# Performance work log

Measured on AMD Instinct MI355X. Metric: run time of the kernel, lower is better.

Reference implementation:

```python
import jax, jax.numpy as jnp
import numpy as np

N_HEAD = 12

def setup_inputs() -> dict:
    key = jax.random.key(0)
    k1, k2, k3, k4, k5 = jax.random.split(key, 5)
    B, T, C = 16, 1024, 768
    s = 0.02
    return {
        "x": jax.random.normal(k1, (B, T, C), dtype=jnp.float32),
        "W_attn": jax.random.normal(k2, (C, 3 * C), dtype=jnp.float32) * s,
        "b_attn": jax.random.normal(k3, (3 * C,), dtype=jnp.float32) * s,
        "W_proj": jax.random.normal(k4, (C, C), dtype=jnp.float32) * s,
        "b_proj": jax.random.normal(k5, (C,), dtype=jnp.float32) * s,
    }

def reference(x, W_attn, b_attn, W_proj, b_proj):
    B, T, C = x.shape
    H = N_HEAD
    d = C // H
    qkv = x @ W_attn + b_attn                      # [B,T,3C]
    q, k, v = jnp.split(qkv, 3, axis=-1)
    # [B,H,T,d]
    q = q.reshape(B, T, H, d).transpose(0, 2, 1, 3)
    k = k.reshape(B, T, H, d).transpose(0, 2, 1, 3)
    v = v.reshape(B, T, H, d).transpose(0, 2, 1, 3)
    scale = 1.0 / jnp.sqrt(jnp.array(d, dtype=x.dtype))
    att = jnp.einsum('bhqd,bhkd->bhqk', q, k) * scale   # [B,H,T,T]
    causal = jnp.tril(jnp.ones((T, T), dtype=bool))
    att = jnp.where(causal[None, None], att, -jnp.inf)
    att = jax.nn.softmax(att, axis=-1)
    # dropout is identity in eval mode (p=0 for deterministic reference)
    y = jnp.einsum('bhqk,bhkd->bhqd', att, v)            # [B,H,T,d]
    y = y.transpose(0, 2, 1, 3).reshape(B, T, C)
    return y @ W_proj + b_proj
```

## Files before the change

### kernel.cpp

```cpp
#include <hip/hip_runtime.h>
#include <cstddef>


typedef __bf16 bf16_t;
typedef __bf16 bf16x4 __attribute__((ext_vector_type(4)));
typedef __bf16 bf16x8 __attribute__((ext_vector_type(8)));
typedef float  f32x4  __attribute__((ext_vector_type(4)));

#define MFMA16(a,b,c) __builtin_amdgcn_mfma_f32_16x16x32_bf16((a),(b),(c),0,0,0)
#define GLOAD16(gp, lp) \
  __builtin_amdgcn_global_load_lds((const __attribute__((address_space(1))) unsigned int*)(gp), \
                                   (__attribute__((address_space(3))) unsigned int*)(lp), 16, 0, 0)

#define SWZ(row, c) (((row) * 64) + ((((c) ^ ((row) & 7)) * 8)))

#define QSCALE 0.1803368801111f

__global__ __launch_bounds__(256)
void xcast_kernel(const float* __restrict__ in, bf16_t* __restrict__ out)
{
    const size_t i = ((size_t)blockIdx.x * 256 + threadIdx.x) * 4;
    float4 f = *(const float4*)(in + i);
    bf16x4 o = {(bf16_t)f.x, (bf16_t)f.y, (bf16_t)f.z, (bf16_t)f.w};
    *(bf16x4*)(out + i) = o;
}

__global__ __launch_bounds__(256)
void tcast_kernel(const float* __restrict__ in, bf16_t* __restrict__ out, int R, int Cn)
{
    __shared__ bf16_t tile[32][33];
    const int tx = threadIdx.x & 31, ty = threadIdx.x >> 5;
    const int c0 = blockIdx.x * 32, r0 = blockIdx.y * 32;
#pragma unroll
    for (int i = 0; i < 4; ++i)
        tile[ty + i*8][tx] = (bf16_t)in[(size_t)(r0 + ty + i*8) * Cn + c0 + tx];
    __syncthreads();
#pragma unroll
    for (int i = 0; i < 4; ++i)
        out[(size_t)(c0 + ty + i*8) * R + r0 + tx] = tile[tx][ty + i*8];
}

#define LGKM0() asm volatile("s_waitcnt lgkmcnt(0)" ::: "memory")
#define VMC(n)  asm volatile("s_waitcnt vmcnt(" #n ")" ::: "memory")
#define PBAR()  __builtin_amdgcn_s_barrier()
#define PRIO1() __builtin_amdgcn_s_setprio(1)
#define PRIO0() __builtin_amdgcn_s_setprio(0)

#define STAGE_HT(buf, kt, ht) do { \
    const int r0_ = w * 16 + (((ht) & 1) ? 128 : 0); \
    if ((ht) < 2) { \
        GLOAD16(WT + (size_t)(nt + r0_ + lr) * 768 + (kt) + lcs,     &Bs[buf][r0_ * 64]); \
        GLOAD16(WT + (size_t)(nt + r0_ + 8 + lr) * 768 + (kt) + lcs, &Bs[buf][(r0_ + 8) * 64]); \
    } else { \
        GLOAD16(Xb + (size_t)(mt + r0_ + lr) * 768 + (kt) + lcs,     &As[buf][r0_ * 64]); \
        GLOAD16(Xb + (size_t)(mt + r0_ + 8 + lr) * 768 + (kt) + lcs, &As[buf][(r0_ + 8) * 64]); \
    } \
} while (0)

#define RD_BX(dst, buf) do { \
    _Pragma("unroll") for (int j_ = 0; j_ < 4; ++j_) \
    _Pragma("unroll") for (int ks_ = 0; ks_ < 2; ++ks_) \
        (dst)[j_][ks_] = *(const bf16x8*)(&As[buf][SWZ(wc * 64 + j_ * 16 + lm, ks_ * 4 + lq)]); \
} while (0)

#define RD_AW(dst, buf, F0, NF) do { \
    _Pragma("unroll") for (int p_ = 0; p_ < (NF); ++p_) \
    _Pragma("unroll") for (int ks_ = 0; ks_ < 2; ++ks_) \
        (dst)[p_][ks_] = *(const bf16x8*)(&Bs[buf][SWZ(wr * 128 + ((F0) + p_) * 16 + lm, ks_ * 4 + lq)]); \
} while (0)

#define MFMA_Q(AW, BX, F0) do { \
    _Pragma("unroll") for (int ks_ = 0; ks_ < 2; ++ks_) \
    _Pragma("unroll") for (int p_ = 0; p_ < 2; ++p_) \
    _Pragma("unroll") for (int j_ = 0; j_ < 4; ++j_) \
        acc[(F0) + p_][j_] = MFMA16((AW)[p_][ks_], (BX)[j_][ks_], acc[(F0) + p_][j_]); \
} while (0)

__global__ __launch_bounds__(512)
void qkv_gemm8(const bf16_t* __restrict__ Xb, const bf16_t* __restrict__ WT,
               const float* __restrict__ bias,
               bf16_t* __restrict__ Qb, bf16_t* __restrict__ Kb, bf16_t* __restrict__ VT)
{
    __shared__ bf16_t As[2][256 * 64];
    __shared__ bf16_t Bs[2][256 * 64];
    const int tid = threadIdx.x;
    const int w = tid >> 6, l = tid & 63;
    const int lm = l & 15, lq = l >> 4;
    const int lr = l >> 3;
    const int lcs = ((l & 7) ^ lr) * 8;
    const int wr = w >> 2, wc = w & 3;

    const int g = blockIdx.x;
    const int gt = (g & 7) * 72 + (g >> 3);
    const int bm = gt / 9, bn = gt % 9;
    const int mt = bm * 256, nt = bn * 256;

    f32x4 acc[8][4];
    const f32x4 z4 = {0.f, 0.f, 0.f, 0.f};
#pragma unroll
    for (int i = 0; i < 8; ++i)
#pragma unroll
        for (int j = 0; j < 4; ++j) acc[i][j] = z4;

    bf16x8 bx0[4][2], bx1[4][2];
    bf16x8 aw0[2][2], aw12[4][2], aw3[2][2];

    STAGE_HT(0, 0, 0); STAGE_HT(0, 0, 1); STAGE_HT(0, 0, 2); STAGE_HT(0, 0, 3);
    STAGE_HT(1, 64, 0); STAGE_HT(1, 64, 1);
    VMC(4);
    PBAR();
    RD_BX(bx0, 0); RD_AW(aw0, 0, 0, 2);

#pragma unroll 1
    for (int it = 0; it < 5; ++it) {
        const int kv = it * 128 + 64, ku2 = kv + 64, kv2 = ku2 + 64;
        RD_AW(aw12, 0, 2, 4);
        STAGE_HT(1, kv, 2);
        PBAR(); LGKM0();
        PRIO1(); MFMA_Q(aw0, bx0, 0); PRIO0();
        PBAR();
        RD_AW(aw3, 0, 6, 2);
        STAGE_HT(1, kv, 3);
        PBAR(); LGKM0();
        PRIO1(); MFMA_Q(aw12, bx0, 2); PRIO0();
        PBAR();
        STAGE_HT(0, ku2, 0);
        PBAR();
        PRIO1(); MFMA_Q(&aw12[2], bx0, 4); PRIO0();
        VMC(2);
        PBAR();
        RD_BX(bx1, 1); RD_AW(aw0, 1, 0, 2);
        STAGE_HT(0, ku2, 1);
        PBAR(); LGKM0();
        PRIO1(); MFMA_Q(aw3, bx0, 6); PRIO0();
        PBAR();
        RD_AW(aw12, 1, 2, 4);
        STAGE_HT(0, ku2, 2);
        PBAR(); LGKM0();
        PRIO1(); MFMA_Q(aw0, bx1, 0); PRIO0();
        PBAR();
        RD_AW(aw3, 1, 6, 2);
        STAGE_HT(0, ku2, 3);
        PBAR(); LGKM0();
        PRIO1(); MFMA_Q(aw12, bx1, 2); PRIO0();
        PBAR();
        STAGE_HT(1, kv2, 0);
        PBAR();
        PRIO1(); MFMA_Q(&aw12[2], bx1, 4); PRIO0();
        VMC(2);
        PBAR();
        RD_BX(bx0, 0); RD_AW(aw0, 0, 0, 2);
        STAGE_HT(1, kv2, 1);
        PBAR(); LGKM0();
        PRIO1(); MFMA_Q(aw3, bx1, 6); PRIO0();
        PBAR();
    }

    RD_AW(aw12, 0, 2, 4);
    STAGE_HT(1, 704, 2);
    PBAR(); LGKM0();
    PRIO1(); MFMA_Q(aw0, bx0, 0); PRIO0();
    PBAR();
    RD_AW(aw3, 0, 6, 2);
    STAGE_HT(1, 704, 3);
    PBAR(); LGKM0();
    PRIO1(); MFMA_Q(aw12, bx0, 2); PRIO0();
    PBAR();
    PRIO1(); MFMA_Q(&aw12[2], bx0, 4); PRIO0();
    VMC(0);
    PBAR();
    RD_BX(bx1, 1); RD_AW(aw0, 1, 0, 2);
    MFMA_Q(aw3, bx0, 6);
    RD_AW(aw12, 1, 2, 4);
    LGKM0();
    MFMA_Q(aw0, bx1, 0);
    MFMA_Q(aw12, bx1, 2);
    RD_AW(aw3, 1, 6, 2);
    LGKM0();
    MFMA_Q(&aw12[2], bx1, 4);
    MFMA_Q(aw3, bx1, 6);

    const int which = (nt) / 768;
    const int b_ = mt >> 10;
    const int tb = (mt & 1023) + wc * 64;
    if (which == 2) {
#pragma unroll
        for (int f = 0; f < 8; ++f) {
            const int nglob = nt + wr * 128 + f * 16 + lq * 4;
            const int nin = nglob - 1536;
            const int h = nin >> 6, d0 = nin & 63;
            bf16_t* vt = VT + (size_t)(b_ * 12 + h) * 65536;
            const float4 bv = *(const float4*)(bias + nglob);
#pragma unroll
            for (int j = 0; j < 4; ++j) {
                const int t = tb + j * 16 + lm;
                f32x4 v = acc[f][j];
                vt[(size_t)(d0 + 0) * 1024 + t] = (bf16_t)(v[0] + bv.x);
                vt[(size_t)(d0 + 1) * 1024 + t] = (bf16_t)(v[1] + bv.y);
                vt[(size_t)(d0 + 2) * 1024 + t] = (bf16_t)(v[2] + bv.z);
                vt[(size_t)(d0 + 3) * 1024 + t] = (bf16_t)(v[3] + bv.w);
            }
        }
    } else {
        bf16_t* dst = (which == 0) ? Qb : Kb;
        const float qs = (which == 0) ? QSCALE : 1.0f;
#pragma unroll
        for (int f = 0; f < 8; ++f) {
            const int nglob = nt + wr * 128 + f * 16 + lq * 4;
            const int nin = nglob - which * 768;
            const int h = nin >> 6, d0 = nin & 63;
            const float4 bv = *(const float4*)(bias + nglob);
#pragma unroll
            for (int j = 0; j < 4; ++j) {
                const int t = tb + j * 16 + lm;
                f32x4 v = acc[f][j];
                bf16x4 o4 = {(bf16_t)((v[0] + bv.x) * qs), (bf16_t)((v[1] + bv.y) * qs),
                             (bf16_t)((v[2] + bv.z) * qs), (bf16_t)((v[3] + bv.w) * qs)};
                *(bf16x4*)(dst + ((size_t)(b_ * 12 + h) * 1024 + t) * 64 + d0) = o4;
            }
        }
    }
}

__global__ __launch_bounds__(256, 3)
void attn_kernel(const bf16_t* __restrict__ Qb, const bf16_t* __restrict__ Kb,
                 const bf16_t* __restrict__ VT, bf16_t* __restrict__ Y)
{
    __shared__ bf16_t Ks[2][64 * 64];
    __shared__ bf16_t Vs[2][64 * 64];
    __shared__ bf16_t Plds[4 * 16 * 72];
    const int tid = threadIdx.x;
    const int w = tid >> 6, l = tid & 63;
    const int lm = l & 15, lq = l >> 4;
    const int lr = l >> 3;
    const int lc8 = ((l & 7) ^ lr) * 8;
    const int xp = blockIdx.x;
    const int bh = blockIdx.y;
    const int loq = xp * 128, hiq = (7 - xp) * 128;

    int qmin[4];
    qmin[0] = loq + w * 32;      qmin[1] = qmin[0] + 16;
    qmin[2] = hiq + w * 32;      qmin[3] = qmin[2] + 16;

    const bf16_t* Kbase = Kb + (size_t)bh * 65536;
    const bf16_t* Vbase = VT + (size_t)bh * 65536;
    bf16_t* Pw = &Plds[w * 1152];
    const int r0a = w * 16, r0b = w * 16 + 8;

    bf16x8 bq[4][2];
#pragma unroll
    for (int m = 0; m < 4; ++m) {
        const bf16_t* Qp = Qb + ((size_t)bh * 1024 + qmin[m] + lm) * 64;
        bq[m][0] = *(const bf16x8*)(Qp + lq * 8);
        bq[m][1] = *(const bf16x8*)(Qp + 32 + lq * 8);
    }

    f32x4 O[4][4];
    float li[4] = {0.f, 0.f, 0.f, 0.f};
    const f32x4 z4 = {0.f, 0.f, 0.f, 0.f};
#pragma unroll
    for (int m = 0; m < 4; ++m)
#pragma unroll
        for (int s = 0; s < 4; ++s) O[m][s] = z4;

    const int kend = hiq + 64;

    GLOAD16(Kbase + (size_t)(r0a + lr) * 64 + lc8,   &Ks[0][r0a * 64]);
    GLOAD16(Kbase + (size_t)(r0b + lr) * 64 + lc8,   &Ks[0][r0b * 64]);
    GLOAD16(Vbase + (size_t)(r0a + lr) * 1024 + lc8, &Vs[0][r0a * 64]);
    GLOAD16(Vbase + (size_t)(r0b + lr) * 1024 + lc8, &Vs[0][r0b * 64]);
    __syncthreads();

    int cb = 0;
    for (int k0 = 0; k0 <= kend; k0 += 64) {
        const int nxt = cb ^ 1;
        if (k0 + 64 <= kend) {
            const int kn = k0 + 64;
            if (nxt) {
                GLOAD16(Kbase + (size_t)(kn + r0a + lr) * 64 + lc8,        &Ks[1][r0a * 64]);
                GLOAD16(Kbase + (size_t)(kn + r0b + lr) * 64 + lc8,        &Ks[1][r0b * 64]);
                GLOAD16(Vbase + (size_t)(r0a + lr) * 1024 + kn + lc8,      &Vs[1][r0a * 64]);
                GLOAD16(Vbase + (size_t)(r0b + lr) * 1024 + kn + lc8,      &Vs[1][r0b * 64]);
            } else {
                GLOAD16(Kbase + (size_t)(kn + r0a + lr) * 64 + lc8,        &Ks[0][r0a * 64]);
                GLOAD16(Kbase + (size_t)(kn + r0b + lr) * 64 + lc8,        &Ks[0][r0b * 64]);
                GLOAD16(Vbase + (size_t)(r0a + lr) * 1024 + kn + lc8,      &Vs[0][r0a * 64]);
                GLOAD16(Vbase + (size_t)(r0b + lr) * 1024 + kn + lc8,      &Vs[0][r0b * 64]);
            }
        }
        const bf16_t* Kc = Ks[cb];
        const bf16_t* Vc = Vs[cb];
#pragma unroll
        for (int m = 0; m < 4; ++m) {
            if (k0 > qmin[m] + 15) continue;
            f32x4 S[4];
#pragma unroll
            for (int s = 0; s < 4; ++s) S[s] = z4;
#pragma unroll
            for (int ks = 0; ks < 2; ++ks)
#pragma unroll
                for (int s = 0; s < 4; ++s) {
                    bf16x8 ak = *(const bf16x8*)(&Kc[SWZ(s * 16 + lm, ks * 4 + lq)]);
                    S[s] = MFMA16(ak, bq[m][ks], S[s]);
                }
            if (k0 + 63 > qmin[m]) {
                const int q = qmin[m] + lm;
#pragma unroll
                for (int s = 0; s < 4; ++s)
#pragma unroll
                    for (int rg = 0; rg < 4; ++rg)
                        if (k0 + s * 16 + lq * 4 + rg > q) S[s][rg] = -1e30f;
            }
            float ls = 0.f;
#pragma unroll
            for (int s = 0; s < 4; ++s)
#pragma unroll
                for (int rg = 0; rg < 4; ++rg) {
                    float pv = exp2f(S[s][rg]);
                    S[s][rg] = pv;
                    ls += pv;
                }
            li[m] += ls;
#pragma unroll
            for (int s = 0; s < 4; ++s) {
                bf16x4 p4 = {(bf16_t)S[s][0], (bf16_t)S[s][1],
                             (bf16_t)S[s][2], (bf16_t)S[s][3]};
                *(bf16x4*)(&Pw[lm * 72 + s * 16 + lq * 4]) = p4;
            }
#pragma unroll
            for (int ks = 0; ks < 2; ++ks) {
                bf16x8 bp = *(const bf16x8*)(&Pw[lm * 72 + ks * 32 + lq * 8]);
#pragma unroll
                for (int s = 0; s < 4; ++s) {
                    bf16x8 av = *(const bf16x8*)(&Vc[SWZ(s * 16 + lm, ks * 4 + lq)]);
                    O[m][s] = MFMA16(av, bp, O[m][s]);
                }
            }
        }
        __syncthreads();
        cb = nxt;
    }

    const int b = bh / 12, h = bh % 12;
#pragma unroll
    for (int m = 0; m < 4; ++m) {
        float s0 = li[m];
        s0 += __shfl_xor(s0, 16, 64);
        s0 += __shfl_xor(s0, 32, 64);
        const float inv = 1.f / s0;
        const size_t row = ((size_t)(b * 1024 + qmin[m] + lm)) * 768 + h * 64;
#pragma unroll
        for (int s = 0; s < 4; ++s) {
            bf16x4 y4 = {(bf16_t)(O[m][s][0] * inv), (bf16_t)(O[m][s][1] * inv),
                         (bf16_t)(O[m][s][2] * inv), (bf16_t)(O[m][s][3] * inv)};
            *(bf16x4*)(Y + row + s * 16 + lq * 4) = y4;
        }
    }
}

__global__ __launch_bounds__(256)
void proj_gemm(const bf16_t* __restrict__ A, const bf16_t* __restrict__ WT,
               const float* __restrict__ bias, float* __restrict__ out)
{
    __shared__ bf16_t As[128 * 64];
    __shared__ bf16_t Bs[128 * 64];
    const int tid = threadIdx.x;
    const int w = tid >> 6, l = tid & 63;
    const int lm = l & 15, lq = l >> 4;
    const int wy = w >> 1, wx = w & 1;
    const int lr = l >> 3;
    const int lcs = ((l & 7) ^ lr) * 8;
    const int nt = blockIdx.x * 128, mt = blockIdx.y * 128;

    f32x4 acc[4][4];
    const f32x4 z4 = {0.f, 0.f, 0.f, 0.f};
#pragma unroll
    for (int i = 0; i < 4; ++i)
#pragma unroll
        for (int j = 0; j < 4; ++j) acc[i][j] = z4;

    for (int kt = 0; kt < 768; kt += 64) {
#pragma unroll
        for (int p = 0; p < 4; ++p) {
            const int row = w * 32 + p * 8;
            GLOAD16(A  + (size_t)(mt + row + lr) * 768 + kt + lcs, &As[row * 64]);
            GLOAD16(WT + (size_t)(nt + row + lr) * 768 + kt + lcs, &Bs[row * 64]);
        }
        __syncthreads();
#pragma unroll
        for (int ks = 0; ks < 2; ++ks) {
            const int c = ks * 4 + lq;
            bf16x8 aw[4], bx[4];
#pragma unroll
            for (int i = 0; i < 4; ++i)
                aw[i] = *(const bf16x8*)(&Bs[SWZ(wx * 64 + i * 16 + lm, c)]);
#pragma unroll
            for (int j = 0; j < 4; ++j)
                bx[j] = *(const bf16x8*)(&As[SWZ(wy * 64 + j * 16 + lm, c)]);
#pragma unroll
            for (int i = 0; i < 4; ++i)
#pragma unroll
                for (int j = 0; j < 4; ++j)
                    acc[i][j] = MFMA16(aw[i], bx[j], acc[i][j]);
        }
        __syncthreads();
    }
#pragma unroll
    for (int i = 0; i < 4; ++i) {
        const int n0 = nt + wx * 64 + i * 16 + lq * 4;
        const float4 bv = *(const float4*)(bias + n0);
#pragma unroll
        for (int j = 0; j < 4; ++j) {
            const int t = mt + wy * 64 + j * 16 + lm;
            f32x4 v = acc[i][j];
            float4 o = {v[0] + bv.x, v[1] + bv.y, v[2] + bv.z, v[3] + bv.w};
            *(float4*)(out + (size_t)t * 768 + n0) = o;
        }
    }
}

extern "C" void kernel_launch(void* const* d_in, const int* in_sizes, int n_in,
                              void* d_out, int out_size, void* d_ws, size_t ws_size,
                              hipStream_t stream)
{
    const float* x      = (const float*)d_in[0];
    const float* W_attn = (const float*)d_in[1];
    const float* b_attn = (const float*)d_in[2];
    const float* W_proj = (const float*)d_in[3];
    const float* b_proj = (const float*)d_in[4];
    float* out = (float*)d_out;

    char* ws = (char*)d_ws;
    const size_t SZ = (size_t)16 * 12 * 1024 * 64 * 2;
    bf16_t* Qb  = (bf16_t*)(ws);
    bf16_t* Kb  = (bf16_t*)(ws + SZ);
    bf16_t* VT  = (bf16_t*)(ws + 3 * SZ);
    bf16_t* Yb  = (bf16_t*)(ws + 4 * SZ);
    bf16_t* Xb  = (bf16_t*)(ws + 4 * SZ);
    bf16_t* WaT = (bf16_t*)(ws + 5 * SZ);
    bf16_t* WpT = (bf16_t*)(ws + 5 * SZ + (size_t)2304 * 768 * 2);

    xcast_kernel<<<12288, 256, 0, stream>>>(x, Xb);
    tcast_kernel<<<dim3(72, 24), 256, 0, stream>>>(W_attn, WaT, 768, 2304);
    tcast_kernel<<<dim3(24, 24), 256, 0, stream>>>(W_proj, WpT, 768, 768);
    qkv_gemm8<<<576, 512, 0, stream>>>(Xb, WaT, b_attn, Qb, Kb, VT);
    attn_kernel<<<dim3(4, 192), 256, 0, stream>>>(Qb, Kb, VT, Yb);
    proj_gemm<<<dim3(6, 128), 256, 0, stream>>>(Yb, WpT, b_proj, out);
}
```

Baseline: 291.6 us.

## Deepen QKV GEMM prefetch to a full tile ahead and simplify the epilogue

The QKV GEMM prologue now loads both K-tiles completely before the loop starts. Inside the loop, each buffer's remaining quarters are restaged with the next K-slice as soon as it has been read, and the vmcnt waits are relaxed so more global-to-LDS loads stay in flight. The loop tail becomes a plain drain of the two resident buffers. `launch_bounds` also gains a minimum-blocks hint of 2, which caps register use and risks spills. The reordered staging could race with LDS reads if the quarter regions overlap.

Result: faster. 285.6 us (-2.1%).

```diff
diff --git a/kernel.cpp b/kernel.cpp
--- a/kernel.cpp
+++ b/kernel.cpp
@@ -76,7 +76,7 @@
         acc[(F0) + p_][j_] = MFMA16((AW)[p_][ks_], (BX)[j_][ks_], acc[(F0) + p_][j_]); \
 } while (0)
 
-__global__ __launch_bounds__(512)
+__global__ __launch_bounds__(512, 2)
 void qkv_gemm8(const bf16_t* __restrict__ Xb, const bf16_t* __restrict__ WT,
                const float* __restrict__ bias,
                bf16_t* __restrict__ Qb, bf16_t* __restrict__ Kb, bf16_t* __restrict__ VT)
@@ -106,28 +106,28 @@
     bf16x8 aw0[2][2], aw12[4][2], aw3[2][2];
 
     STAGE_HT(0, 0, 0); STAGE_HT(0, 0, 1); STAGE_HT(0, 0, 2); STAGE_HT(0, 0, 3);
-    STAGE_HT(1, 64, 0); STAGE_HT(1, 64, 1);
-    VMC(4);
+    STAGE_HT(1, 64, 0); STAGE_HT(1, 64, 1); STAGE_HT(1, 64, 2); STAGE_HT(1, 64, 3);
+    VMC(8);
     PBAR();
     RD_BX(bx0, 0); RD_AW(aw0, 0, 0, 2);
 
 #pragma unroll 1
     for (int it = 0; it < 5; ++it) {
-        const int kv = it * 128 + 64, ku2 = kv + 64, kv2 = ku2 + 64;
+        const int ku2 = it * 128 + 128, kv2 = it * 128 + 192;
         RD_AW(aw12, 0, 2, 4);
-        STAGE_HT(1, kv, 2);
+        STAGE_HT(0, ku2, 2);
         PBAR(); LGKM0();
         PRIO1(); MFMA_Q(aw0, bx0, 0); PRIO0();
         PBAR();
         RD_AW(aw3, 0, 6, 2);
-        STAGE_HT(1, kv, 3);
+        STAGE_HT(0, ku2, 3);
         PBAR(); LGKM0();
         PRIO1(); MFMA_Q(aw12, bx0, 2); PRIO0();
         PBAR();
         STAGE_HT(0, ku2, 0);
         PBAR();
         PRIO1(); MFMA_Q(&aw12[2], bx0, 4); PRIO0();
-        VMC(2);
+        VMC(6);
         PBAR();
         RD_BX(bx1, 1); RD_AW(aw0, 1, 0, 2);
         STAGE_HT(0, ku2, 1);
@@ -135,19 +135,19 @@
         PRIO1(); MFMA_Q(aw3, bx0, 6); PRIO0();
         PBAR();
         RD_AW(aw12, 1, 2, 4);
-        STAGE_HT(0, ku2, 2);
+        STAGE_HT(1, kv2, 2);
         PBAR(); LGKM0();
         PRIO1(); MFMA_Q(aw0, bx1, 0); PRIO0();
         PBAR();
         RD_AW(aw3, 1, 6, 2);
-        STAGE_HT(0, ku2, 3);
+        STAGE_HT(1, kv2, 3);
         PBAR(); LGKM0();
         PRIO1(); MFMA_Q(aw12, bx1, 2); PRIO0();
         PBAR();
         STAGE_HT(1, kv2, 0);
         PBAR();
         PRIO1(); MFMA_Q(&aw12[2], bx1, 4); PRIO0();
-        VMC(2);
+        VMC(6);
         PBAR();
         RD_BX(bx0, 0); RD_AW(aw0, 0, 0, 2);
         STAGE_HT(1, kv2, 1);
@@ -156,29 +156,15 @@
         PBAR();
     }
 
-    RD_AW(aw12, 0, 2, 4);
-    STAGE_HT(1, 704, 2);
-    PBAR(); LGKM0();
-    PRIO1(); MFMA_Q(aw0, bx0, 0); PRIO0();
-    PBAR();
-    RD_AW(aw3, 0, 6, 2);
-    STAGE_HT(1, 704, 3);
-    PBAR(); LGKM0();
-    PRIO1(); MFMA_Q(aw12, bx0, 2); PRIO0();
-    PBAR();
-    PRIO1(); MFMA_Q(&aw12[2], bx0, 4); PRIO0();
     VMC(0);
     PBAR();
+    RD_AW(aw12, 0, 2, 4); RD_AW(aw3, 0, 6, 2);
+    MFMA_Q(aw0, bx0, 0); MFMA_Q(aw12, bx0, 2);
+    MFMA_Q(&aw12[2], bx0, 4); MFMA_Q(aw3, bx0, 6);
     RD_BX(bx1, 1); RD_AW(aw0, 1, 0, 2);
-    MFMA_Q(aw3, bx0, 6);
-    RD_AW(aw12, 1, 2, 4);
-    LGKM0();
-    MFMA_Q(aw0, bx1, 0);
-    MFMA_Q(aw12, bx1, 2);
-    RD_AW(aw3, 1, 6, 2);
-    LGKM0();
-    MFMA_Q(&aw12[2], bx1, 4);
-    MFMA_Q(aw3, bx1, 6);
+    RD_AW(aw12, 1, 2, 4); RD_AW(aw3, 1, 6, 2);
+    MFMA_Q(aw0, bx1, 0); MFMA_Q(aw12, bx1, 2);
+    MFMA_Q(&aw12[2], bx1, 4); MFMA_Q(aw3, bx1, 6);
 
     const int which = (nt) / 768;
     const int b_ = mt >> 10;
```

## Read K and V fragments directly from global memory in attention kernel

Applied to the files above, without the earlier changes.

Removes the LDS double-buffered K/V staging and block-wide barriers, so each wave loads its MFMA operands for K and transposed V straight from global memory. The loop order is swapped to iterate per query group with a per-group causal key bound, which removes the shared-loop skip checks. This gives up data sharing across the four waves through LDS, so each wave now issues its own global and L2 reads, which raises memory traffic and exposes load latency without explicit prefetching.

After: 444.1 us. 52.3% more time.

```diff
diff --git a/kernel.cpp b/kernel.cpp
--- a/kernel.cpp
+++ b/kernel.cpp
@@ -226,14 +226,10 @@
 void attn_kernel(const bf16_t* __restrict__ Qb, const bf16_t* __restrict__ Kb,
                  const bf16_t* __restrict__ VT, bf16_t* __restrict__ Y)
 {
-    __shared__ bf16_t Ks[2][64 * 64];
-    __shared__ bf16_t Vs[2][64 * 64];
     __shared__ bf16_t Plds[4 * 16 * 72];
     const int tid = threadIdx.x;
     const int w = tid >> 6, l = tid & 63;
     const int lm = l & 15, lq = l >> 4;
-    const int lr = l >> 3;
-    const int lc8 = ((l & 7) ^ lr) * 8;
     const int xp = blockIdx.x;
     const int bh = blockIdx.y;
     const int loq = xp * 128, hiq = (7 - xp) * 128;
@@ -245,7 +241,6 @@
     const bf16_t* Kbase = Kb + (size_t)bh * 65536;
     const bf16_t* Vbase = VT + (size_t)bh * 65536;
     bf16_t* Pw = &Plds[w * 1152];
-    const int r0a = w * 16, r0b = w * 16 + 8;
 
     bf16x8 bq[4][2];
 #pragma unroll
@@ -263,36 +258,19 @@
 #pragma unroll
         for (int s = 0; s < 4; ++s) O[m][s] = z4;
 
-    const int kend = hiq + 64;
-
-    GLOAD16(Kbase + (size_t)(r0a + lr) * 64 + lc8,   &Ks[0][r0a * 64]);
-    GLOAD16(Kbase + (size_t)(r0b + lr) * 64 + lc8,   &Ks[0][r0b * 64]);
-    GLOAD16(Vbase + (size_t)(r0a + lr) * 1024 + lc8, &Vs[0][r0a * 64]);
-    GLOAD16(Vbase + (size_t)(r0b + lr) * 1024 + lc8, &Vs[0][r0b * 64]);
-    __syncthreads();
-
-    int cb = 0;
-    for (int k0 = 0; k0 <= kend; k0 += 64) {
-        const int nxt = cb ^ 1;
-        if (k0 + 64 <= kend) {
-            const int kn = k0 + 64;
-            if (nxt) {
-                GLOAD16(Kbase + (size_t)(kn + r0a + lr) * 64 + lc8,        &Ks[1][r0a * 64]);
-                GLOAD16(Kbase + (size_t)(kn + r0b + lr) * 64 + lc8,        &Ks[1][r0b * 64]);
-                GLOAD16(Vbase + (size_t)(r0a + lr) * 1024 + kn + lc8,      &Vs[1][r0a * 64]);
-                GLOAD16(Vbase + (size_t)(r0b + lr) * 1024 + kn + lc8,      &Vs[1][r0b * 64]);
-            } else {
-                GLOAD16(Kbase + (size_t)(kn + r0a + lr) * 64 + lc8,        &Ks[0][r0a * 64]);
-                GLOAD16(Kbase + (size_t)(kn + r0b + lr) * 64 + lc8,        &Ks[0][r0b * 64]);
-                GLOAD16(Vbase + (size_t)(r0a + lr) * 1024 + kn + lc8,      &Vs[0][r0a * 64]);
-                GLOAD16(Vbase + (size_t)(r0b + lr) * 1024 + kn + lc8,      &Vs[0][r0b * 64]);
-            }
-        }
-        const bf16_t* Kc = Ks[cb];
-        const bf16_t* Vc = Vs[cb];
-#pragma unroll
-        for (int m = 0; m < 4; ++m) {
-            if (k0 > qmin[m] + 15) continue;
+#pragma unroll 1
+    for (int m = 0; m < 4; ++m) {
+        const int qm = qmin[m];
+        const int q = qm + lm;
+#pragma unroll 1
+        for (int k0 = 0; k0 < qm + 16; k0 += 64) {
+            bf16x8 av[2][4];
+#pragma unroll
+            for (int ks = 0; ks < 2; ++ks)
+#pragma unroll
+                for (int s = 0; s < 4; ++s)
+                    av[ks][s] = *(const bf16x8*)(Vbase + (size_t)(s * 16 + lm) * 1024
+                                                 + k0 + ks * 32 + lq * 8);
             f32x4 S[4];
 #pragma unroll
             for (int s = 0; s < 4; ++s) S[s] = z4;
@@ -300,11 +278,11 @@
             for (int ks = 0; ks < 2; ++ks)
 #pragma unroll
                 for (int s = 0; s < 4; ++s) {
-                    bf16x8 ak = *(const bf16x8*)(&Kc[SWZ(s * 16 + lm, ks * 4 + lq)]);
+                    bf16x8 ak = *(const bf16x8*)(Kbase + (size_t)(k0 + s * 16 + lm) * 64
+                                                 + ks * 32 + lq * 8);
                     S[s] = MFMA16(ak, bq[m][ks], S[s]);
                 }
-            if (k0 + 63 > qmin[m]) {
-                const int q = qmin[m] + lm;
+            if (k0 + 63 > qm) {
 #pragma unroll
                 for (int s = 0; s < 4; ++s)
 #pragma unroll
@@ -331,14 +309,10 @@
             for (int ks = 0; ks < 2; ++ks) {
                 bf16x8 bp = *(const bf16x8*)(&Pw[lm * 72 + ks * 32 + lq * 8]);
 #pragma unroll
-                for (int s = 0; s < 4; ++s) {
-                    bf16x8 av = *(const bf16x8*)(&Vc[SWZ(s * 16 + lm, ks * 4 + lq)]);
-                    O[m][s] = MFMA16(av, bp, O[m][s]);
-                }
+                for (int s = 0; s < 4; ++s)
+                    O[m][s] = MFMA16(av[ks][s], bp, O[m][s]);
             }
         }
-        __syncthreads();
-        cb = nxt;
     }
 
     const int b = bh / 12, h = bh % 12;
```
